# Kernel tuning notes

Measured on AMD Instinct MI355X. Metric: run time of the kernel, lower is better.

## Reference

```python
import jax, jax.numpy as jnp
import numpy as np

NUM_EXPERTS = 16
TOP_K = 2
AUX_LOSS_COEF = 0.01


def setup_inputs() -> dict:
    key = jax.random.key(0)
    ks = jax.random.split(key, 5)
    B, S, D, I, E = 4, 2048, 1024, 2816, NUM_EXPERTS
    scale = 0.02
    return {
        "x": jax.random.normal(ks[0], (B, S, D), dtype=jnp.float32),
        "gate_w": jax.random.normal(ks[1], (D, E), dtype=jnp.float32) * scale,
        "Wg": jax.random.normal(ks[2], (E, D, I), dtype=jnp.float32) * scale,
        "Wu": jax.random.normal(ks[3], (E, D, I), dtype=jnp.float32) * scale,
        "Wd": jax.random.normal(ks[4], (E, I, D), dtype=jnp.float32) * scale,
    }


def _moe_forward(x, gate_w, Wg, Wu, Wd):
    B, S, D = x.shape
    E = gate_w.shape[1]
    # Router
    logits = x @ gate_w                      # [B,S,E]
    probs = jax.nn.softmax(logits, axis=-1)  # [B,S,E]
    topk_w, topk_idx = jax.lax.top_k(probs, TOP_K)        # [B,S,K]
    topk_w = topk_w / jnp.sum(topk_w, axis=-1, keepdims=True)
    # Per-token combine weight for each expert: [B,S,E]
    onehot = jax.nn.one_hot(topk_idx, E, dtype=x.dtype)   # [B,S,K,E]
    combine_w = jnp.einsum("bsk,bske->bse", topk_w, onehot)
    x_flat = x.reshape(-1, D)                # [T,D]
    w_flat = combine_w.reshape(-1, E)        # [T,E]
    # Accumulate weighted expert outputs (loop over fixed small E; unselected
    # tokens get zero weight, identical math to masked gather/scatter).
    out = jnp.zeros_like(x_flat)
    for e in range(E):
        h = jax.nn.silu(x_flat @ Wg[e]) * (x_flat @ Wu[e])  # [T,I]
        out = out + (h @ Wd[e]) * w_flat[:, e:e + 1]
    out = out.reshape(B, S, D)
    # Load balancing aux loss
    expert_mask = onehot.sum(axis=2)                        # [B,S,E]
    tokens_per_expert = expert_mask.mean(axis=(0, 1))       # [E]
    router_prob_per_expert = probs.mean(axis=(0, 1))        # [E]
    aux_loss = AUX_LOSS_COEF * jnp.sum(tokens_per_expert * router_prob_per_expert) * E
    return out, aux_loss


def reference(x, gate_w, Wg, Wu, Wd):
    return _moe_forward(x, gate_w, Wg, Wu, Wd)
```

## Files before the change

kernel.cpp:

```cpp
#include <hip/hip_runtime.h>
#include <stdint.h>

#define T_TOKENS 8192
#define D_DIM 1024
#define I_DIM 2816
#define E_NUM 16
#define N_SLOTS 16384

typedef float f32x4 __attribute__((ext_vector_type(4)));
typedef short s16x8 __attribute__((ext_vector_type(8)));
typedef short s16x4 __attribute__((ext_vector_type(4)));
typedef unsigned short u16;
typedef unsigned int u32;

__device__ __forceinline__ u16 f2bf(float f) {
  u32 u = __builtin_bit_cast(u32, f);
  u = (u + 0x7FFFu + ((u >> 16) & 1u)) >> 16;
  return (u16)u;
}
__device__ __forceinline__ u32 pack2(float a, float b) {
  return (u32)f2bf(a) | ((u32)f2bf(b) << 16);
}
__device__ __forceinline__ void async_load16(const void* g, void* l) {
  __builtin_amdgcn_global_load_lds(
      (const __attribute__((address_space(1))) void*)g,
      (__attribute__((address_space(3))) void*)l, 16, 0, 0);
}

__global__ void router_kernel(const float* __restrict__ x,
                              const float* __restrict__ gw,
                              int* __restrict__ e12, float* __restrict__ w12,
                              int* __restrict__ cnt, float* __restrict__ probsum) {
  __shared__ float sProb[E_NUM];
  __shared__ int sCnt[E_NUM];
  int tid = threadIdx.x;
  if (tid < E_NUM) { sProb[tid] = 0.f; sCnt[tid] = 0; }
  __syncthreads();
  int g = tid >> 4, i = tid & 15;
  int t = blockIdx.x * 16 + g;
  float acc[E_NUM];
#pragma unroll
  for (int e = 0; e < E_NUM; e++) acc[e] = 0.f;
  const f32x4* x4 = (const f32x4*)(x + (size_t)t * D_DIM);
  const f32x4* g4 = (const f32x4*)gw;
  for (int jj = 0; jj < 16; jj++) {
    f32x4 xv = x4[i + 16 * jj];
    int jb = 4 * (i + 16 * jj);
#pragma unroll
    for (int r = 0; r < 4; r++) {
      float xs = xv[r];
#pragma unroll
      for (int e4 = 0; e4 < 4; e4++) {
        f32x4 gv = g4[(jb + r) * 4 + e4];
        acc[e4 * 4 + 0] += xs * gv[0];
        acc[e4 * 4 + 1] += xs * gv[1];
        acc[e4 * 4 + 2] += xs * gv[2];
        acc[e4 * 4 + 3] += xs * gv[3];
      }
    }
  }
#pragma unroll
  for (int e = 0; e < E_NUM; e++) {
    float v = acc[e];
    v += __shfl_down(v, 8, 16);
    v += __shfl_down(v, 4, 16);
    v += __shfl_down(v, 2, 16);
    v += __shfl_down(v, 1, 16);
    acc[e] = v;
  }
  if (i == 0) {
    float mx = acc[0];
#pragma unroll
    for (int e = 1; e < E_NUM; e++) mx = fmaxf(mx, acc[e]);
    float p[E_NUM]; float s = 0.f;
#pragma unroll
    for (int e = 0; e < E_NUM; e++) { p[e] = __expf(acc[e] - mx); s += p[e]; }
    float inv = 1.f / s;
#pragma unroll
    for (int e = 0; e < E_NUM; e++) p[e] *= inv;
    int e1 = 0; float p1 = p[0];
#pragma unroll
    for (int e = 1; e < E_NUM; e++) if (p[e] > p1) { p1 = p[e]; e1 = e; }
    int e2 = (e1 == 0) ? 1 : 0; float p2 = p[e2];
#pragma unroll
    for (int e = 0; e < E_NUM; e++) if (e != e1 && p[e] > p2) { p2 = p[e]; e2 = e; }
    float wsum = p1 + p2;
    e12[2 * t] = e1; e12[2 * t + 1] = e2;
    w12[2 * t] = p1 / wsum; w12[2 * t + 1] = p2 / wsum;
#pragma unroll
    for (int e = 0; e < E_NUM; e++) atomicAdd(&sProb[e], p[e]);
    atomicAdd(&sCnt[e1], 1);
    atomicAdd(&sCnt[e2], 1);
  }
  __syncthreads();
  if (tid < E_NUM) {
    atomicAdd(&cnt[tid], sCnt[tid]);
    atomicAdd(&probsum[tid], sProb[tid]);
  }
}

__global__ void prefix_kernel(const int* __restrict__ cnt, int* __restrict__ offsets,
                              const float* __restrict__ probsum, float* __restrict__ aux_out) {
  if (threadIdx.x == 0) {
    int s = 0;
    for (int e = 0; e < E_NUM; e++) { offsets[e] = s; s += cnt[e]; }
    offsets[E_NUM] = s;
    float a = 0.f;
    for (int e = 0; e < E_NUM; e++) a += (float)cnt[e] * probsum[e];
    aux_out[0] = 0.01f * 16.f * a / (8192.f * 8192.f);
  }
}

__global__ void build_kernel(const int* __restrict__ e12, const float* __restrict__ w12,
                             const int* __restrict__ offsets, int* __restrict__ cursor,
                             int* __restrict__ tlist, float* __restrict__ wlist,
                             int* __restrict__ slot2) {
  int t = blockIdx.x * 256 + threadIdx.x;
  if (t >= T_TOKENS) return;
#pragma unroll
  for (int k = 0; k < 2; k++) {
    int e = e12[2 * t + k];
    int pos = atomicAdd(&cursor[e], 1);
    int idx = offsets[e] + pos;
    tlist[idx] = t;
    wlist[idx] = w12[2 * t + k];
    slot2[2 * t + k] = idx;
  }
}

__global__ void gather_kernel(const float* __restrict__ x, const int* __restrict__ tlist,
                              u16* __restrict__ Xe) {
  int r = blockIdx.x * 4 + (threadIdx.x >> 6);
  int lane = threadIdx.x & 63;
  int tok = tlist[r];
  const f32x4* src = (const f32x4*)(x + (size_t)tok * D_DIM);
  u32* dst = (u32*)(Xe + (size_t)r * D_DIM);
#pragma unroll
  for (int c = 0; c < 4; c++) {
    f32x4 v = src[lane + 64 * c];
    dst[(lane + 64 * c) * 2] = pack2(v[0], v[1]);
    dst[(lane + 64 * c) * 2 + 1] = pack2(v[2], v[3]);
  }
}

template <int K, int N>
__global__ __launch_bounds__(256) void transpose_kernel(const float* __restrict__ W,
                                                        u16* __restrict__ Wt) {
  __shared__ u16 tile[64][258];
  int e = blockIdx.z;
  int k0 = blockIdx.x * 64;
  int n0 = blockIdx.y * 256;
  const float* Win = W + (size_t)e * K * N;
  u16* Wout = Wt + (size_t)e * N * K;
  int t = threadIdx.x;
  int r = t >> 4;
  int c4 = (t & 15) * 4;
#pragma unroll
  for (int rep = 0; rep < 4; rep++) {
    int k = r + rep * 16;
    const float* rowp = Win + (size_t)(k0 + k) * N + n0;
#pragma unroll
    for (int s = 0; s < 4; s++) {
      f32x4 v = *(const f32x4*)(rowp + s * 64 + c4);
      *(u32*)&tile[k][s * 64 + c4] = pack2(v[0], v[1]);
      *(u32*)&tile[k][s * 64 + c4 + 2] = pack2(v[2], v[3]);
    }
  }
  __syncthreads();
#pragma unroll
  for (int rep = 0; rep < 8; rep++) {
    int c = t + 256 * rep;
    int n = c >> 3;
    int k8 = (c & 7) * 8;
    s16x8 o;
#pragma unroll
    for (int i = 0; i < 8; i++) o[i] = tile[k8 + i][n];
    *(s16x8*)(Wout + (size_t)(n0 + n) * K + k0 + k8) = o;
  }
}

__global__ __launch_bounds__(512, 2) void gemm_gu_kernel(
    const u16* __restrict__ Abuf, const u16* __restrict__ Bg, const u16* __restrict__ Bu,
    u16* __restrict__ Hbuf,
    const int* __restrict__ cnt, const int* __restrict__ offsets) {
  int e = blockIdx.z;
  int Me = cnt[e];
  int m0 = blockIdx.y * 256;
  if (m0 >= Me) return;
  int n0 = blockIdx.x * 128;
  int rowBase = offsets[e];
  const u16* Bge = Bg + (size_t)e * I_DIM * D_DIM;
  const u16* Bue = Bu + (size_t)e * I_DIM * D_DIM;

  __shared__ u16 lds[65536];
  constexpr int A0 = 0, A1 = 16384;
  constexpr int Bg0 = 32768, Bg1 = 40960;
  constexpr int Bu0 = 49152, Bu1 = 57344;

  int tid = threadIdx.x;
  int lane = tid & 63;
  int wv = tid >> 6;
  int wm = wv >> 1;
  int wn = wv & 1;
  int lrow = lane & 15, lq = lane >> 4;
  int swz = lrow & 7;

  f32x4 accg[4][4], accu[4][4];
#pragma unroll
  for (int a = 0; a < 4; a++)
#pragma unroll
    for (int b = 0; b < 4; b++) { accg[a][b] = (f32x4)0.f; accu[a][b] = (f32x4)0.f; }

  auto STAGE = [&](int kt, int b) {
    int k0 = kt << 6;
#pragma unroll
    for (int r = 0; r < 4; r++) {
      int c = tid + 512 * r;
      int row = c >> 3, slot = c & 7;
      int gr = m0 + row; gr = (gr < Me) ? gr : (Me - 1);
      const u16* src = Abuf + (size_t)(rowBase + gr) * D_DIM + k0 + ((slot ^ (row & 7)) << 3);
      async_load16(src, (void*)&lds[(b ? A1 : A0) + (wv * 64 + 512 * r) * 8]);
    }
#pragma unroll
    for (int r = 0; r < 2; r++) {
      int c = tid + 512 * r;
      int row = c >> 3, slot = c & 7;
      int col = k0 + ((slot ^ (row & 7)) << 3);
      int ldso = (wv * 64 + 512 * r) * 8;
      async_load16(Bge + (size_t)(n0 + row) * D_DIM + col, (void*)&lds[(b ? Bg1 : Bg0) + ldso]);
      async_load16(Bue + (size_t)(n0 + row) * D_DIM + col, (void*)&lds[(b ? Bu1 : Bu0) + ldso]);
    }
  };

  STAGE(0, 0);
  STAGE(1, 1);

  for (int kt = 0; kt < 16; kt++) {
    int cur = kt & 1;
    if (kt < 15) asm volatile("s_waitcnt vmcnt(8)");
    else         asm volatile("s_waitcnt vmcnt(0)");
    __builtin_amdgcn_s_barrier();
    __builtin_amdgcn_sched_barrier(0);

    const u16* As = lds + (cur ? A1 : A0);
    const u16* Bgs = lds + (cur ? Bg1 : Bg0);
    const u16* Bus = lds + (cur ? Bu1 : Bu0);

#pragma unroll
    for (int kh = 0; kh < 2; kh++) {
      s16x8 af[4], bb[4];
      int so = ((kh * 4 + lq) ^ swz) << 3;
#pragma unroll
      for (int fm = 0; fm < 4; fm++) {
        int row = wm * 64 + fm * 16 + lrow;
        af[fm] = *(const s16x8*)&As[row * 64 + so];
      }
#pragma unroll
      for (int fn = 0; fn < 4; fn++) {
        int row = wn * 64 + fn * 16 + lrow;
        bb[fn] = *(const s16x8*)&Bgs[row * 64 + so];
      }
      __builtin_amdgcn_s_barrier();
      __builtin_amdgcn_s_setprio(1);
#pragma unroll
      for (int fm = 0; fm < 4; fm++)
#pragma unroll
        for (int fn = 0; fn < 4; fn++)
          accg[fm][fn] = __builtin_amdgcn_mfma_f32_16x16x32_bf16(af[fm], bb[fn], accg[fm][fn], 0, 0, 0);
      __builtin_amdgcn_s_setprio(0);
      __builtin_amdgcn_s_barrier();
#pragma unroll
      for (int fn = 0; fn < 4; fn++) {
        int row = wn * 64 + fn * 16 + lrow;
        bb[fn] = *(const s16x8*)&Bus[row * 64 + so];
      }
      __builtin_amdgcn_s_barrier();
      __builtin_amdgcn_s_setprio(1);
#pragma unroll
      for (int fm = 0; fm < 4; fm++)
#pragma unroll
        for (int fn = 0; fn < 4; fn++)
          accu[fm][fn] = __builtin_amdgcn_mfma_f32_16x16x32_bf16(af[fm], bb[fn], accu[fm][fn], 0, 0, 0);
      __builtin_amdgcn_s_setprio(0);
      __builtin_amdgcn_s_barrier();
    }

    __builtin_amdgcn_sched_barrier(0);
    if (kt + 2 < 16) STAGE(kt + 2, cur);
  }

#pragma unroll
  for (int fm = 0; fm < 4; fm++) {
#pragma unroll
    for (int i = 0; i < 4; i++) {
      int m = m0 + wm * 64 + fm * 16 + lq * 4 + i;
      if (m >= Me) continue;
      size_t arow = (size_t)(rowBase + m);
#pragma unroll
      for (int fn = 0; fn < 4; fn++) {
        int col = n0 + wn * 64 + fn * 16 + lrow;
        float g = accg[fm][fn][i];
        float u = accu[fm][fn][i];
        float h = (g / (1.f + __expf(-g))) * u;
        Hbuf[arow * I_DIM + col] = f2bf(h);
      }
    }
  }
}

__global__ __launch_bounds__(512, 2) void gemm_down_kernel(
    const u16* __restrict__ Abuf, const u16* __restrict__ Bd, float* __restrict__ Y,
    const int* __restrict__ cnt, const int* __restrict__ offsets,
    const float* __restrict__ wlist) {
  int e = blockIdx.z;
  int Me = cnt[e];
  int m0 = blockIdx.y * 256;
  if (m0 >= Me) return;
  int n0 = blockIdx.x * 128;
  int rowBase = offsets[e];
  const u16* Bde = Bd + (size_t)e * D_DIM * I_DIM;

  __shared__ u16 lds[49152];
  constexpr int A0 = 0, A1 = 16384;
  constexpr int B0 = 32768, B1 = 40960;

  int tid = threadIdx.x;
  int lane = tid & 63;
  int wv = tid >> 6;
  int wm = wv >> 1;
  int wn = wv & 1;
  int lrow = lane & 15, lq = lane >> 4;
  int swz = lrow & 7;

  f32x4 acc[4][4];
#pragma unroll
  for (int a = 0; a < 4; a++)
#pragma unroll
    for (int b = 0; b < 4; b++) acc[a][b] = (f32x4)0.f;

  auto STAGE = [&](int kt, int b) {
    int k0 = kt << 6;
#pragma unroll
    for (int r = 0; r < 4; r++) {
      int c = tid + 512 * r;
      int row = c >> 3, slot = c & 7;
      int gr = m0 + row; gr = (gr < Me) ? gr : (Me - 1);
      const u16* src = Abuf + (size_t)(rowBase + gr) * I_DIM + k0 + ((slot ^ (row & 7)) << 3);
      async_load16(src, (void*)&lds[(b ? A1 : A0) + (wv * 64 + 512 * r) * 8]);
    }
    {
      int r = 0;
#pragma unroll
      for (r = 0; r < 2; r++) {
        int c = tid + 512 * r;
        int row = c >> 3, slot = c & 7;
        int col = k0 + ((slot ^ (row & 7)) << 3);
        async_load16(Bde + (size_t)(n0 + row) * I_DIM + col,
                     (void*)&lds[(b ? B1 : B0) + (wv * 64 + 512 * r) * 8]);
      }
    }
  };

  STAGE(0, 0);
  STAGE(1, 1);

  for (int kt = 0; kt < 44; kt++) {
    int cur = kt & 1;
    if (kt < 43) asm volatile("s_waitcnt vmcnt(6)");
    else         asm volatile("s_waitcnt vmcnt(0)");
    __builtin_amdgcn_s_barrier();
    __builtin_amdgcn_sched_barrier(0);

    const u16* As = lds + (cur ? A1 : A0);
    const u16* Bs = lds + (cur ? B1 : B0);

#pragma unroll
    for (int kh = 0; kh < 2; kh++) {
      s16x8 af[4], bb[4];
      int so = ((kh * 4 + lq) ^ swz) << 3;
#pragma unroll
      for (int fm = 0; fm < 4; fm++) {
        int row = wm * 64 + fm * 16 + lrow;
        af[fm] = *(const s16x8*)&As[row * 64 + so];
      }
#pragma unroll
      for (int fn = 0; fn < 4; fn++) {
        int row = wn * 64 + fn * 16 + lrow;
        bb[fn] = *(const s16x8*)&Bs[row * 64 + so];
      }
      __builtin_amdgcn_s_barrier();
      __builtin_amdgcn_s_setprio(1);
#pragma unroll
      for (int fm = 0; fm < 4; fm++)
#pragma unroll
        for (int fn = 0; fn < 4; fn++)
          acc[fm][fn] = __builtin_amdgcn_mfma_f32_16x16x32_bf16(af[fm], bb[fn], acc[fm][fn], 0, 0, 0);
      __builtin_amdgcn_s_setprio(0);
      __builtin_amdgcn_s_barrier();
    }

    __builtin_amdgcn_sched_barrier(0);
    if (kt + 2 < 44) STAGE(kt + 2, cur);
  }

#pragma unroll
  for (int fm = 0; fm < 4; fm++) {
#pragma unroll
    for (int i = 0; i < 4; i++) {
      int m = m0 + wm * 64 + fm * 16 + lq * 4 + i;
      if (m >= Me) continue;
      size_t arow = (size_t)(rowBase + m);
      float w = wlist[arow];
#pragma unroll
      for (int fn = 0; fn < 4; fn++) {
        int col = n0 + wn * 64 + fn * 16 + lrow;
        Y[arow * D_DIM + col] = acc[fm][fn][i] * w;
      }
    }
  }
}

__global__ __launch_bounds__(256) void combine_kernel(
    const float* __restrict__ Y, const int* __restrict__ slot2,
    float* __restrict__ out) {
  int t = blockIdx.x;
  int tid = threadIdx.x;
  int s1 = slot2[2 * t];
  int s2 = slot2[2 * t + 1];
  const f32x4* y1 = (const f32x4*)(Y + (size_t)s1 * D_DIM);
  const f32x4* y2 = (const f32x4*)(Y + (size_t)s2 * D_DIM);
  f32x4* o = (f32x4*)(out + (size_t)t * D_DIM);
  o[tid] = y1[tid] + y2[tid];
}

extern "C" void kernel_launch(void* const* d_in, const int* in_sizes, int n_in,
                              void* d_out, int out_size, void* d_ws, size_t ws_size,
                              hipStream_t stream) {
  const float* x  = (const float*)d_in[0];
  const float* gw = (const float*)d_in[1];
  const float* Wg = (const float*)d_in[2];
  const float* Wu = (const float*)d_in[3];
  const float* Wd = (const float*)d_in[4];
  float* outf = (float*)d_out;
  char* ws = (char*)d_ws;
  int*   cnt     = (int*)(ws + 0);
  int*   cursor  = (int*)(ws + 64);
  float* probsum = (float*)(ws + 128);
  int*   offsets = (int*)(ws + 192);
  int*   e12     = (int*)(ws + 512);
  float* w12     = (float*)(ws + 66048);
  int*   tlist   = (int*)(ws + 131584);
  float* wlist   = (float*)(ws + 197120);
  int*   slot2   = (int*)(ws + 262656);
  u16*   Xe      = (u16*)(ws + (1 << 20));
  u16*   H       = (u16*)(ws + 34603008);
  u16*   WtA     = (u16*)(ws + 134217728);
  u16*   WtB     = (u16*)(ws + 234881024);
  float* Y       = (float*)(ws + 234881024);

  hipMemsetAsync(d_ws, 0, 512, stream);

  router_kernel<<<512, 256, 0, stream>>>(x, gw, e12, w12, cnt, probsum);
  prefix_kernel<<<1, 64, 0, stream>>>(cnt, offsets, probsum, outf + (size_t)(T_TOKENS * D_DIM));
  build_kernel<<<32, 256, 0, stream>>>(e12, w12, offsets, cursor, tlist, wlist, slot2);
  gather_kernel<<<4096, 256, 0, stream>>>(x, tlist, Xe);

  transpose_kernel<D_DIM, I_DIM><<<dim3(16, 11, E_NUM), 256, 0, stream>>>(Wg, WtA);
  transpose_kernel<D_DIM, I_DIM><<<dim3(16, 11, E_NUM), 256, 0, stream>>>(Wu, WtB);

  gemm_gu_kernel<<<dim3(22, 32, E_NUM), 512, 0, stream>>>(Xe, WtA, WtB, H, cnt, offsets);

  transpose_kernel<I_DIM, D_DIM><<<dim3(44, 4, E_NUM), 256, 0, stream>>>(Wd, WtA);

  gemm_down_kernel<<<dim3(8, 32, E_NUM), 512, 0, stream>>>(H, WtA, Y, cnt, offsets, wlist);

  combine_kernel<<<T_TOKENS, 256, 0, stream>>>(Y, slot2, outf);
}
```

Before: 1.134 ms.

## Shrink GEMM tiles to 128x128 with single-buffered synchronous LDS loads

Both expert GEMM kernels go from 512-thread blocks with 256x128 tiles and a double-buffered async LDS pipeline to 256-thread blocks with 128x128 tiles, loading each K-slab and waiting with __syncthreads before compute. The priority and barrier interleaving around the MFMAs is dropped, and the grid doubles in the M dimension. This lowers LDS use per block so more blocks can be resident, and it reduces padding waste for experts whose token counts are not multiples of 256. In exchange, global loads no longer overlap with compute inside a block, and each tile has less data reuse.

```diff
diff --git a/kernel.cpp b/kernel.cpp
--- a/kernel.cpp
+++ b/kernel.cpp
@@ -179,23 +179,22 @@
   }
 }
 
-__global__ __launch_bounds__(512, 2) void gemm_gu_kernel(
+__global__ __launch_bounds__(256, 2) void gemm_gu_kernel(
     const u16* __restrict__ Abuf, const u16* __restrict__ Bg, const u16* __restrict__ Bu,
     u16* __restrict__ Hbuf,
     const int* __restrict__ cnt, const int* __restrict__ offsets) {
   int e = blockIdx.z;
   int Me = cnt[e];
-  int m0 = blockIdx.y * 256;
+  int m0 = blockIdx.y * 128;
   if (m0 >= Me) return;
   int n0 = blockIdx.x * 128;
   int rowBase = offsets[e];
   const u16* Bge = Bg + (size_t)e * I_DIM * D_DIM;
   const u16* Bue = Bu + (size_t)e * I_DIM * D_DIM;
 
-  __shared__ u16 lds[65536];
-  constexpr int A0 = 0, A1 = 16384;
-  constexpr int Bg0 = 32768, Bg1 = 40960;
-  constexpr int Bu0 = 49152, Bu1 = 57344;
+  __shared__ u16 Ash[128 * 64];
+  __shared__ u16 Bgsh[128 * 64];
+  __shared__ u16 Bush[128 * 64];
 
   int tid = threadIdx.x;
   int lane = tid & 63;
@@ -211,82 +210,39 @@
 #pragma unroll
     for (int b = 0; b < 4; b++) { accg[a][b] = (f32x4)0.f; accu[a][b] = (f32x4)0.f; }
 
-  auto STAGE = [&](int kt, int b) {
+  for (int kt = 0; kt < 16; kt++) {
     int k0 = kt << 6;
 #pragma unroll
     for (int r = 0; r < 4; r++) {
-      int c = tid + 512 * r;
+      int c = tid + 256 * r;
       int row = c >> 3, slot = c & 7;
+      int co = (slot ^ (row & 7)) << 3;
+      int ldso = (wv * 64 + 256 * r) * 8;
       int gr = m0 + row; gr = (gr < Me) ? gr : (Me - 1);
-      const u16* src = Abuf + (size_t)(rowBase + gr) * D_DIM + k0 + ((slot ^ (row & 7)) << 3);
-      async_load16(src, (void*)&lds[(b ? A1 : A0) + (wv * 64 + 512 * r) * 8]);
-    }
-#pragma unroll
-    for (int r = 0; r < 2; r++) {
-      int c = tid + 512 * r;
-      int row = c >> 3, slot = c & 7;
-      int col = k0 + ((slot ^ (row & 7)) << 3);
-      int ldso = (wv * 64 + 512 * r) * 8;
-      async_load16(Bge + (size_t)(n0 + row) * D_DIM + col, (void*)&lds[(b ? Bg1 : Bg0) + ldso]);
-      async_load16(Bue + (size_t)(n0 + row) * D_DIM + col, (void*)&lds[(b ? Bu1 : Bu0) + ldso]);
-    }
-  };
-
-  STAGE(0, 0);
-  STAGE(1, 1);
-
-  for (int kt = 0; kt < 16; kt++) {
-    int cur = kt & 1;
-    if (kt < 15) asm volatile("s_waitcnt vmcnt(8)");
-    else         asm volatile("s_waitcnt vmcnt(0)");
-    __builtin_amdgcn_s_barrier();
-    __builtin_amdgcn_sched_barrier(0);
-
-    const u16* As = lds + (cur ? A1 : A0);
-    const u16* Bgs = lds + (cur ? Bg1 : Bg0);
-    const u16* Bus = lds + (cur ? Bu1 : Bu0);
-
+      async_load16(Abuf + (size_t)(rowBase + gr) * D_DIM + k0 + co, &Ash[ldso]);
+      async_load16(Bge + (size_t)(n0 + row) * D_DIM + k0 + co, &Bgsh[ldso]);
+      async_load16(Bue + (size_t)(n0 + row) * D_DIM + k0 + co, &Bush[ldso]);
+    }
+    __syncthreads();
 #pragma unroll
     for (int kh = 0; kh < 2; kh++) {
-      s16x8 af[4], bb[4];
+      s16x8 af[4], bg[4], bu[4];
       int so = ((kh * 4 + lq) ^ swz) << 3;
 #pragma unroll
-      for (int fm = 0; fm < 4; fm++) {
-        int row = wm * 64 + fm * 16 + lrow;
-        af[fm] = *(const s16x8*)&As[row * 64 + so];
-      }
-#pragma unroll
-      for (int fn = 0; fn < 4; fn++) {
-        int row = wn * 64 + fn * 16 + lrow;
-        bb[fn] = *(const s16x8*)&Bgs[row * 64 + so];
-      }
-      __builtin_amdgcn_s_barrier();
-      __builtin_amdgcn_s_setprio(1);
+      for (int f = 0; f < 4; f++) {
+        af[f] = *(const s16x8*)&Ash[(wm * 64 + f * 16 + lrow) * 64 + so];
+        bg[f] = *(const s16x8*)&Bgsh[(wn * 64 + f * 16 + lrow) * 64 + so];
+        bu[f] = *(const s16x8*)&Bush[(wn * 64 + f * 16 + lrow) * 64 + so];
+      }
 #pragma unroll
       for (int fm = 0; fm < 4; fm++)
 #pragma unroll
-        for (int fn = 0; fn < 4; fn++)
-          accg[fm][fn] = __builtin_amdgcn_mfma_f32_16x16x32_bf16(af[fm], bb[fn], accg[fm][fn], 0, 0, 0);
-      __builtin_amdgcn_s_setprio(0);
-      __builtin_amdgcn_s_barrier();
-#pragma unroll
-      for (int fn = 0; fn < 4; fn++) {
-        int row = wn * 64 + fn * 16 + lrow;
-        bb[fn] = *(const s16x8*)&Bus[row * 64 + so];
-      }
-      __builtin_amdgcn_s_barrier();
-      __builtin_amdgcn_s_setprio(1);
-#pragma unroll
-      for (int fm = 0; fm < 4; fm++)
-#pragma unroll
-        for (int fn = 0; fn < 4; fn++)
-          accu[fm][fn] = __builtin_amdgcn_mfma_f32_16x16x32_bf16(af[fm], bb[fn], accu[fm][fn], 0, 0, 0);
-      __builtin_amdgcn_s_setprio(0);
-      __builtin_amdgcn_s_barrier();
-    }
-
-    __builtin_amdgcn_sched_barrier(0);
-    if (kt + 2 < 16) STAGE(kt + 2, cur);
+        for (int fn = 0; fn < 4; fn++) {
+          accg[fm][fn] = __builtin_amdgcn_mfma_f32_16x16x32_bf16(af[fm], bg[fn], accg[fm][fn], 0, 0, 0);
+          accu[fm][fn] = __builtin_amdgcn_mfma_f32_16x16x32_bf16(af[fm], bu[fn], accu[fm][fn], 0, 0, 0);
+        }
+    }
+    __syncthreads();
   }
 
 #pragma unroll
@@ -308,21 +264,20 @@
   }
 }
 
-__global__ __launch_bounds__(512, 2) void gemm_down_kernel(
+__global__ __launch_bounds__(256, 3) void gemm_down_kernel(
     const u16* __restrict__ Abuf, const u16* __restrict__ Bd, float* __restrict__ Y,
     const int* __restrict__ cnt, const int* __restrict__ offsets,
     const float* __restrict__ wlist) {
   int e = blockIdx.z;
   int Me = cnt[e];
-  int m0 = blockIdx.y * 256;
+  int m0 = blockIdx.y * 128;
   if (m0 >= Me) return;
   int n0 = blockIdx.x * 128;
   int rowBase = offsets[e];
   const u16* Bde = Bd + (size_t)e * D_DIM * I_DIM;
 
-  __shared__ u16 lds[49152];
-  constexpr int A0 = 0, A1 = 16384;
-  constexpr int B0 = 32768, B1 = 40960;
+  __shared__ u16 Ash[128 * 64];
+  __shared__ u16 Bsh[128 * 64];
 
   int tid = threadIdx.x;
   int lane = tid & 63;
@@ -338,69 +293,35 @@
 #pragma unroll
     for (int b = 0; b < 4; b++) acc[a][b] = (f32x4)0.f;
 
-  auto STAGE = [&](int kt, int b) {
+  for (int kt = 0; kt < 44; kt++) {
     int k0 = kt << 6;
 #pragma unroll
     for (int r = 0; r < 4; r++) {
-      int c = tid + 512 * r;
+      int c = tid + 256 * r;
       int row = c >> 3, slot = c & 7;
+      int co = (slot ^ (row & 7)) << 3;
+      int ldso = (wv * 64 + 256 * r) * 8;
       int gr = m0 + row; gr = (gr < Me) ? gr : (Me - 1);
-      const u16* src = Abuf + (size_t)(rowBase + gr) * I_DIM + k0 + ((slot ^ (row & 7)) << 3);
-      async_load16(src, (void*)&lds[(b ? A1 : A0) + (wv * 64 + 512 * r) * 8]);
-    }
-    {
-      int r = 0;
-#pragma unroll
-      for (r = 0; r < 2; r++) {
-        int c = tid + 512 * r;
-        int row = c >> 3, slot = c & 7;
-        int col = k0 + ((slot ^ (row & 7)) << 3);
-        async_load16(Bde + (size_t)(n0 + row) * I_DIM + col,
-                     (void*)&lds[(b ? B1 : B0) + (wv * 64 + 512 * r) * 8]);
-      }
-    }
-  };
-
-  STAGE(0, 0);
-  STAGE(1, 1);
-
-  for (int kt = 0; kt < 44; kt++) {
-    int cur = kt & 1;
-    if (kt < 43) asm volatile("s_waitcnt vmcnt(6)");
-    else         asm volatile("s_waitcnt vmcnt(0)");
-    __builtin_amdgcn_s_barrier();
-    __builtin_amdgcn_sched_barrier(0);
-
-    const u16* As = lds + (cur ? A1 : A0);
-    const u16* Bs = lds + (cur ? B1 : B0);
-
+      async_load16(Abuf + (size_t)(rowBase + gr) * I_DIM + k0 + co, &Ash[ldso]);
+      async_load16(Bde + (size_t)(n0 + row) * I_DIM + k0 + co, &Bsh[ldso]);
+    }
+    __syncthreads();
 #pragma unroll
     for (int kh = 0; kh < 2; kh++) {
       s16x8 af[4], bb[4];
       int so = ((kh * 4 + lq) ^ swz) << 3;
 #pragma unroll
-      for (int fm = 0; fm < 4; fm++) {
-        int row = wm * 64 + fm * 16 + lrow;
-        af[fm] = *(const s16x8*)&As[row * 64 + so];
-      }
-#pragma unroll
-      for (int fn = 0; fn < 4; fn++) {
-        int row = wn * 64 + fn * 16 + lrow;
-        bb[fn] = *(const s16x8*)&Bs[row * 64 + so];
-      }
-      __builtin_amdgcn_s_barrier();
-      __builtin_amdgcn_s_setprio(1);
+      for (int f = 0; f < 4; f++) {
+        af[f] = *(const s16x8*)&Ash[(wm * 64 + f * 16 + lrow) * 64 + so];
+        bb[f] = *(const s16x8*)&Bsh[(wn * 64 + f * 16 + lrow) * 64 + so];
+      }
 #pragma unroll
       for (int fm = 0; fm < 4; fm++)
 #pragma unroll
         for (int fn = 0; fn < 4; fn++)
           acc[fm][fn] = __builtin_amdgcn_mfma_f32_16x16x32_bf16(af[fm], bb[fn], acc[fm][fn], 0, 0, 0);
-      __builtin_amdgcn_s_setprio(0);
-      __builtin_amdgcn_s_barrier();
-    }
-
-    __builtin_amdgcn_sched_barrier(0);
-    if (kt + 2 < 44) STAGE(kt + 2, cur);
+    }
+    __syncthreads();
   }
 
 #pragma unroll
@@ -468,11 +389,11 @@
   transpose_kernel<D_DIM, I_DIM><<<dim3(16, 11, E_NUM), 256, 0, stream>>>(Wg, WtA);
   transpose_kernel<D_DIM, I_DIM><<<dim3(16, 11, E_NUM), 256, 0, stream>>>(Wu, WtB);
 
-  gemm_gu_kernel<<<dim3(22, 32, E_NUM), 512, 0, stream>>>(Xe, WtA, WtB, H, cnt, offsets);
+  gemm_gu_kernel<<<dim3(22, 64, E_NUM), 256, 0, stream>>>(Xe, WtA, WtB, H, cnt, offsets);
 
   transpose_kernel<I_DIM, D_DIM><<<dim3(44, 4, E_NUM), 256, 0, stream>>>(Wd, WtA);
 
-  gemm_down_kernel<<<dim3(8, 32, E_NUM), 512, 0, stream>>>(H, WtA, Y, cnt, offsets, wlist);
+  gemm_down_kernel<<<dim3(8, 64, E_NUM), 256, 0, stream>>>(H, WtA, Y, cnt, offsets, wlist);
 
   combine_kernel<<<T_TOKENS, 256, 0, stream>>>(Y, slot2, outf);
 }
```

Measured after the change: 1.090 ms. -3.9%, faster.
